# Kernel optimization log

Hardware: AMD Instinct MI355X
Metric: run time of the kernel (lower is better)

## Reference

```python
import jax, jax.numpy as jnp
import numpy as np

GAMMA = 2.0
EPS = 1e-05
B, C = 65536, 1024

def setup_inputs() -> dict:
    key = jax.random.key(0)
    k1, k2 = jax.random.split(key)
    inp = jax.random.normal(k1, (B, C), dtype=jnp.float32)
    target = jax.random.randint(k2, (B,), 0, C, dtype=jnp.int64)
    return {"input": inp, "target": target}

def reference(input, target):
    # input: (B, C) float32, target: (B,) int
    target = target.reshape(-1)
    n_cls = input.shape[1]
    # per-class histogram (replaces python loop of C boolean-sum reductions)
    counts = jnp.zeros((n_cls,), dtype=jnp.float32).at[target].add(1.0)
    c = counts.min() / counts + EPS  # (C,)
    # stable softmax/log-softmax, single pass
    logpt = jax.nn.log_softmax(input, axis=-1)  # (B, C)
    pt = jnp.exp(logpt)
    # gather target column only
    rows = jnp.arange(input.shape[0])
    pt_t = pt[rows, target]        # (B,)
    logpt_t = logpt[rows, target]  # (B,)
    loss = -((1.0 - pt_t) ** GAMMA) * logpt_t * c[target]
    return loss.mean()
```

## Files before the change

### kernel.cpp

```cpp
#include <hip/hip_runtime.h>

#define NCLS 1024
#define EPS_C 1e-5f
#define LOSS_BLOCKS 2048

__global__ __launch_bounds__(1024) void hist_weights_kernel(const int* __restrict__ tgt,
                                                            float* __restrict__ w,
                                                            int B) {
    __shared__ unsigned int h[NCLS];
    __shared__ float smin[16];
    const int tid = threadIdx.x;
    h[tid] = 0u;
    __syncthreads();

    const int4* t4 = (const int4*)tgt;
    const int n4 = B >> 2;
    for (int i = tid; i < n4; i += 1024) {
        int4 v = t4[i];
        atomicAdd(&h[v.x & (NCLS - 1)], 1u);
        atomicAdd(&h[v.y & (NCLS - 1)], 1u);
        atomicAdd(&h[v.z & (NCLS - 1)], 1u);
        atomicAdd(&h[v.w & (NCLS - 1)], 1u);
    }
    __syncthreads();

    float c = (float)h[tid];
    float m = c;
    #pragma unroll
    for (int off = 32; off > 0; off >>= 1) m = fminf(m, __shfl_xor(m, off));
    if ((tid & 63) == 0) smin[tid >> 6] = m;
    __syncthreads();
    if (tid == 0) {
        float mm = smin[0];
        #pragma unroll
        for (int i = 1; i < 16; ++i) mm = fminf(mm, smin[i]);
        smin[0] = mm;
    }
    __syncthreads();
    w[tid] = smin[0] / c + EPS_C;
}

__device__ __forceinline__ float sumexp16(float4 a, float4 b, float4 c, float4 d) {
    return __expf(a.x) + __expf(a.y) + __expf(a.z) + __expf(a.w)
         + __expf(b.x) + __expf(b.y) + __expf(b.z) + __expf(b.w)
         + __expf(c.x) + __expf(c.y) + __expf(c.z) + __expf(c.w)
         + __expf(d.x) + __expf(d.y) + __expf(d.z) + __expf(d.w);
}

__global__ __launch_bounds__(256) void loss_kernel(const float* __restrict__ inp,
                                                   const int* __restrict__ tgt,
                                                   const float* __restrict__ w,
                                                   float* __restrict__ partials,
                                                   int B) {
    const int wave  = threadIdx.x >> 6;
    const int lane  = threadIdx.x & 63;
    const int gwave = blockIdx.x * 4 + wave;
    const int base  = gwave * 8;

    float acc = 0.0f;

    if (base + 8 <= B) {
        float s[8];
        const float4* rp = (const float4*)(inp + (size_t)base * NCLS);
        #pragma unroll
        for (int rr = 0; rr < 8; ++rr) {
            float4 a0 = rp[lane];
            float4 a1 = rp[lane + 64];
            float4 a2 = rp[lane + 128];
            float4 a3 = rp[lane + 192];
            s[rr] = sumexp16(a0, a1, a2, a3);
            rp += NCLS / 4;
        }
        #pragma unroll
        for (int off = 32; off > 0; off >>= 1) {
            #pragma unroll
            for (int rr = 0; rr < 8; ++rr) s[rr] += __shfl_xor(s[rr], off);
        }
        float myS = s[0];
        #pragma unroll
        for (int rr = 1; rr < 8; ++rr) myS = (lane == rr) ? s[rr] : myS;

        float l = 0.0f;
        if (lane < 8) {
            const int row = base + lane;
            const int t = tgt[row] & (NCLS - 1);
            const float xt = inp[(size_t)row * NCLS + t];
            const float lp = xt - __logf(myS);
            const float p  = __expf(lp);
            const float o  = 1.0f - p;
            l = -o * o * lp * w[t];
        }
        l += __shfl_xor(l, 1);
        l += __shfl_xor(l, 2);
        l += __shfl_xor(l, 4);
        acc = l;
    } else {
        for (int r = base; r < B && r < base + 8; ++r) {
            const float4* rp = (const float4*)(inp + (size_t)r * NCLS);
            float4 a0 = rp[lane], a1 = rp[lane + 64], a2 = rp[lane + 128], a3 = rp[lane + 192];
            float s0 = sumexp16(a0, a1, a2, a3);
            #pragma unroll
            for (int off = 32; off > 0; off >>= 1) s0 += __shfl_xor(s0, off);
            const int t = tgt[r] & (NCLS - 1);
            const float xt = inp[(size_t)r * NCLS + t];
            const float lp = xt - __logf(s0);
            const float p  = __expf(lp);
            const float o  = 1.0f - p;
            acc += -o * o * lp * w[t];
        }
    }

    __shared__ float sm[4];
    if (lane == 0) sm[wave] = acc;
    __syncthreads();
    if (threadIdx.x == 0)
        partials[blockIdx.x] = sm[0] + sm[1] + sm[2] + sm[3];
}

__global__ __launch_bounds__(1024) void reduce_finalize(const float* __restrict__ partials,
                                                        float* __restrict__ out,
                                                        int n, float invB) {
    __shared__ float sm[16];
    float s = 0.0f;
    for (int i = threadIdx.x; i < n; i += 1024) s += partials[i];
    #pragma unroll
    for (int off = 32; off > 0; off >>= 1) s += __shfl_xor(s, off);
    if ((threadIdx.x & 63) == 0) sm[threadIdx.x >> 6] = s;
    __syncthreads();
    if (threadIdx.x == 0) {
        float t = 0.0f;
        #pragma unroll
        for (int i = 0; i < 16; ++i) t += sm[i];
        out[0] = t * invB;
    }
}

extern "C" void kernel_launch(void* const* d_in, const int* in_sizes, int n_in,
                              void* d_out, int out_size, void* d_ws, size_t ws_size,
                              hipStream_t stream) {
    const float* inp = (const float*)d_in[0];
    const int*   tgt = (const int*)d_in[1];
    const int B = in_sizes[1];

    float* w        = (float*)d_ws;
    float* partials = (float*)((char*)d_ws + 4096);

    hist_weights_kernel<<<1, 1024, 0, stream>>>(tgt, w, B);
    loss_kernel<<<LOSS_BLOCKS, 256, 0, stream>>>(inp, tgt, w, partials, B);
    reduce_finalize<<<1, 1024, 0, stream>>>(partials, (float*)d_out,
                                            LOSS_BLOCKS, 1.0f / (float)B);
}
```

Baseline: 53.66 us.

## Fold class histogram into loss kernel via per-class atomic bins

Removes the separate single-block histogram kernel. The loss kernel now accumulates the unweighted focal term and a count per target class with global atomics, and a finalize kernel derives the class weights from the counts and forms the weighted sum. The goal is to drop the serial single-block histogram pass that runs before the bandwidth-bound loss pass. In exchange it adds a memset and many global atomics on 1024 bins, which can contend and makes the float summation order nondeterministic.

Result: slower. 56.77 us (+5.8%).

```diff
diff --git a/kernel.cpp b/kernel.cpp
--- a/kernel.cpp
+++ b/kernel.cpp
@@ -3,42 +3,6 @@
 #define NCLS 1024
 #define EPS_C 1e-5f
 #define LOSS_BLOCKS 2048
-
-__global__ __launch_bounds__(1024) void hist_weights_kernel(const int* __restrict__ tgt,
-                                                            float* __restrict__ w,
-                                                            int B) {
-    __shared__ unsigned int h[NCLS];
-    __shared__ float smin[16];
-    const int tid = threadIdx.x;
-    h[tid] = 0u;
-    __syncthreads();
-
-    const int4* t4 = (const int4*)tgt;
-    const int n4 = B >> 2;
-    for (int i = tid; i < n4; i += 1024) {
-        int4 v = t4[i];
-        atomicAdd(&h[v.x & (NCLS - 1)], 1u);
-        atomicAdd(&h[v.y & (NCLS - 1)], 1u);
-        atomicAdd(&h[v.z & (NCLS - 1)], 1u);
-        atomicAdd(&h[v.w & (NCLS - 1)], 1u);
-    }
-    __syncthreads();
-
-    float c = (float)h[tid];
-    float m = c;
-    #pragma unroll
-    for (int off = 32; off > 0; off >>= 1) m = fminf(m, __shfl_xor(m, off));
-    if ((tid & 63) == 0) smin[tid >> 6] = m;
-    __syncthreads();
-    if (tid == 0) {
-        float mm = smin[0];
-        #pragma unroll
-        for (int i = 1; i < 16; ++i) mm = fminf(mm, smin[i]);
-        smin[0] = mm;
-    }
-    __syncthreads();
-    w[tid] = smin[0] / c + EPS_C;
-}
 
 __device__ __forceinline__ float sumexp16(float4 a, float4 b, float4 c, float4 d) {
     return __expf(a.x) + __expf(a.y) + __expf(a.z) + __expf(a.w)
@@ -49,15 +13,14 @@
 
 __global__ __launch_bounds__(256) void loss_kernel(const float* __restrict__ inp,
                                                    const int* __restrict__ tgt,
-                                                   const float* __restrict__ w,
-                                                   float* __restrict__ partials,
+                                                   float* __restrict__ fbins,
+                                                   unsigned int* __restrict__ cbins,
                                                    int B) {
     const int wave  = threadIdx.x >> 6;
     const int lane  = threadIdx.x & 63;
     const int gwave = blockIdx.x * 4 + wave;
     const int base  = gwave * 8;
-
-    float acc = 0.0f;
+    if (base >= B) return;
 
     if (base + 8 <= B) {
         float s[8];
@@ -80,7 +43,6 @@
         #pragma unroll
         for (int rr = 1; rr < 8; ++rr) myS = (lane == rr) ? s[rr] : myS;
 
-        float l = 0.0f;
         if (lane < 8) {
             const int row = base + lane;
             const int t = tgt[row] & (NCLS - 1);
@@ -88,12 +50,10 @@
             const float lp = xt - __logf(myS);
             const float p  = __expf(lp);
             const float o  = 1.0f - p;
-            l = -o * o * lp * w[t];
+            const float f  = -o * o * lp;
+            atomicAdd(&fbins[t], f);
+            atomicAdd(&cbins[t], 1u);
         }
-        l += __shfl_xor(l, 1);
-        l += __shfl_xor(l, 2);
-        l += __shfl_xor(l, 4);
-        acc = l;
     } else {
         for (int r = base; r < B && r < base + 8; ++r) {
             const float4* rp = (const float4*)(inp + (size_t)r * NCLS);
@@ -101,36 +61,51 @@
             float s0 = sumexp16(a0, a1, a2, a3);
             #pragma unroll
             for (int off = 32; off > 0; off >>= 1) s0 += __shfl_xor(s0, off);
-            const int t = tgt[r] & (NCLS - 1);
-            const float xt = inp[(size_t)r * NCLS + t];
-            const float lp = xt - __logf(s0);
-            const float p  = __expf(lp);
-            const float o  = 1.0f - p;
-            acc += -o * o * lp * w[t];
+            if (lane == 0) {
+                const int t = tgt[r] & (NCLS - 1);
+                const float xt = inp[(size_t)r * NCLS + t];
+                const float lp = xt - __logf(s0);
+                const float p  = __expf(lp);
+                const float o  = 1.0f - p;
+                atomicAdd(&fbins[t], -o * o * lp);
+                atomicAdd(&cbins[t], 1u);
+            }
         }
     }
-
-    __shared__ float sm[4];
-    if (lane == 0) sm[wave] = acc;
-    __syncthreads();
-    if (threadIdx.x == 0)
-        partials[blockIdx.x] = sm[0] + sm[1] + sm[2] + sm[3];
 }
 
-__global__ __launch_bounds__(1024) void reduce_finalize(const float* __restrict__ partials,
-                                                        float* __restrict__ out,
-                                                        int n, float invB) {
-    __shared__ float sm[16];
-    float s = 0.0f;
-    for (int i = threadIdx.x; i < n; i += 1024) s += partials[i];
+__global__ __launch_bounds__(1024) void finalize_kernel(const float* __restrict__ fbins,
+                                                        const unsigned int* __restrict__ cbins,
+                                                        float* __restrict__ out, float invB) {
+    __shared__ float sred[16];
+    const int tid = threadIdx.x;
+    const unsigned int cu = cbins[tid];
+    const float c = (float)cu;
+
+    float m = c;
     #pragma unroll
-    for (int off = 32; off > 0; off >>= 1) s += __shfl_xor(s, off);
-    if ((threadIdx.x & 63) == 0) sm[threadIdx.x >> 6] = s;
+    for (int off = 32; off > 0; off >>= 1) m = fminf(m, __shfl_xor(m, off));
+    if ((tid & 63) == 0) sred[tid >> 6] = m;
     __syncthreads();
-    if (threadIdx.x == 0) {
+    if (tid == 0) {
+        float mm = sred[0];
+        #pragma unroll
+        for (int i = 1; i < 16; ++i) mm = fminf(mm, sred[i]);
+        sred[0] = mm;
+    }
+    __syncthreads();
+    const float cmin = sred[0];
+    __syncthreads();
+
+    float v = (cu > 0u) ? fbins[tid] * (cmin / c + EPS_C) : 0.0f;
+    #pragma unroll
+    for (int off = 32; off > 0; off >>= 1) v += __shfl_xor(v, off);
+    if ((tid & 63) == 0) sred[tid >> 6] = v;
+    __syncthreads();
+    if (tid == 0) {
         float t = 0.0f;
         #pragma unroll
-        for (int i = 0; i < 16; ++i) t += sm[i];
+        for (int i = 0; i < 16; ++i) t += sred[i];
         out[0] = t * invB;
     }
 }
@@ -142,11 +117,11 @@
     const int*   tgt = (const int*)d_in[1];
     const int B = in_sizes[1];
 
-    float* w        = (float*)d_ws;
-    float* partials = (float*)((char*)d_ws + 4096);
+    unsigned int* cbins = (unsigned int*)d_ws;
+    float*        fbins = (float*)((char*)d_ws + 4096);
 
-    hist_weights_kernel<<<1, 1024, 0, stream>>>(tgt, w, B);
-    loss_kernel<<<LOSS_BLOCKS, 256, 0, stream>>>(inp, tgt, w, partials, B);
-    reduce_finalize<<<1, 1024, 0, stream>>>(partials, (float*)d_out,
-                                            LOSS_BLOCKS, 1.0f / (float)B);
+    hipMemsetAsync(d_ws, 0, 8192, stream);
+
+    loss_kernel<<<LOSS_BLOCKS, 256, 0, stream>>>(inp, tgt, fbins, cbins, B);
+    finalize_kernel<<<1, 1024, 0, stream>>>(fbins, cbins, (float*)d_out, 1.0f / (float)B);
 }
```

## Split histogram across blocks with per-wave privatized shared bins

Applied to the files above, without the earlier changes.

The single-block histogram kernel becomes a 16-block kernel. Each wave keeps its own private shared-memory histogram to cut atomic contention, and each block writes its partial counts to workspace. A new single-block kernel sums the partials and computes the class weights. This adds one kernel launch. The tail path in the loss kernel is also changed so only lane 0 accumulates per-row loss, which fixes double-counting there.

Measured after the change: 53.36 us. About the same (-0.6%).

```diff
diff --git a/kernel.cpp b/kernel.cpp
--- a/kernel.cpp
+++ b/kernel.cpp
@@ -3,28 +3,44 @@
 #define NCLS 1024
 #define EPS_C 1e-5f
 #define LOSS_BLOCKS 2048
+#define HIST_BLOCKS 16
 
-__global__ __launch_bounds__(1024) void hist_weights_kernel(const int* __restrict__ tgt,
-                                                            float* __restrict__ w,
-                                                            int B) {
-    __shared__ unsigned int h[NCLS];
-    __shared__ float smin[16];
+__global__ __launch_bounds__(1024) void hist_parts_kernel(const int* __restrict__ tgt,
+                                                          unsigned int* __restrict__ parts,
+                                                          int B) {
+    __shared__ unsigned int h[16][NCLS];
     const int tid = threadIdx.x;
-    h[tid] = 0u;
+    const int wv  = tid >> 6;
+    #pragma unroll
+    for (int i = 0; i < 16; ++i) h[i][tid] = 0u;
     __syncthreads();
 
     const int4* t4 = (const int4*)tgt;
     const int n4 = B >> 2;
-    for (int i = tid; i < n4; i += 1024) {
+    for (int i = blockIdx.x * 1024 + tid; i < n4; i += HIST_BLOCKS * 1024) {
         int4 v = t4[i];
-        atomicAdd(&h[v.x & (NCLS - 1)], 1u);
-        atomicAdd(&h[v.y & (NCLS - 1)], 1u);
-        atomicAdd(&h[v.z & (NCLS - 1)], 1u);
-        atomicAdd(&h[v.w & (NCLS - 1)], 1u);
+        atomicAdd(&h[wv][v.x & (NCLS - 1)], 1u);
+        atomicAdd(&h[wv][v.y & (NCLS - 1)], 1u);
+        atomicAdd(&h[wv][v.z & (NCLS - 1)], 1u);
+        atomicAdd(&h[wv][v.w & (NCLS - 1)], 1u);
     }
     __syncthreads();
 
-    float c = (float)h[tid];
+    unsigned int cu = 0;
+    #pragma unroll
+    for (int i = 0; i < 16; ++i) cu += h[i][tid];
+    parts[blockIdx.x * NCLS + tid] = cu;
+}
+
+__global__ __launch_bounds__(1024) void weights_kernel(const unsigned int* __restrict__ parts,
+                                                       float* __restrict__ w) {
+    __shared__ float smin[16];
+    const int tid = threadIdx.x;
+    unsigned int cu = 0;
+    #pragma unroll
+    for (int k = 0; k < HIST_BLOCKS; ++k) cu += parts[k * NCLS + tid];
+    const float c = (float)cu;
+
     float m = c;
     #pragma unroll
     for (int off = 32; off > 0; off >>= 1) m = fminf(m, __shfl_xor(m, off));
@@ -106,7 +122,7 @@
             const float lp = xt - __logf(s0);
             const float p  = __expf(lp);
             const float o  = 1.0f - p;
-            acc += -o * o * lp * w[t];
+            if (lane == 0) acc += -o * o * lp * w[t];
         }
     }
 
@@ -142,10 +158,12 @@
     const int*   tgt = (const int*)d_in[1];
     const int B = in_sizes[1];
 
-    float* w        = (float*)d_ws;
-    float* partials = (float*)((char*)d_ws + 4096);
+    float*        w        = (float*)d_ws;
+    float*        partials = (float*)((char*)d_ws + 4096);
+    unsigned int* parts    = (unsigned int*)((char*)d_ws + 16384);
 
-    hist_weights_kernel<<<1, 1024, 0, stream>>>(tgt, w, B);
+    hist_parts_kernel<<<HIST_BLOCKS, 1024, 0, stream>>>(tgt, parts, B);
+    weights_kernel<<<1, 1024, 0, stream>>>(parts, w);
     loss_kernel<<<LOSS_BLOCKS, 256, 0, stream>>>(inp, tgt, w, partials, B);
     reduce_finalize<<<1, 1024, 0, stream>>>(partials, (float*)d_out,
                                             LOSS_BLOCKS, 1.0f / (float)B);
```
